# Performance work log

Hardware: AMD Instinct MI355X
Metric: run time of the kernel (lower is better)

## Reference

```python
import jax, jax.numpy as jnp
import numpy as np

N_QUBITS = 12
N_LAYERS = 3
N_PARAMS = N_QUBITS * 3 * N_LAYERS  # 108
BATCH = 8192
DIM = 1 << N_QUBITS  # 4096


def _rx(theta):
    c = jnp.cos(theta / 2).astype(jnp.complex64)
    s = jnp.sin(theta / 2).astype(jnp.complex64)
    return jnp.stack([jnp.stack([c, -1j * s]), jnp.stack([-1j * s, c])])


def _ry(theta):
    c = jnp.cos(theta / 2).astype(jnp.complex64)
    s = jnp.sin(theta / 2).astype(jnp.complex64)
    return jnp.stack([jnp.stack([c, -s]), jnp.stack([s, c])])


def _rz(theta):
    e = jnp.exp(-1j * theta.astype(jnp.complex64) / 2)
    z = jnp.zeros((), jnp.complex64)
    return jnp.stack([jnp.stack([e, z]), jnp.stack([z, jnp.conj(e)])])


def _apply_1q(state, q, U):
    # state: (B,) + (2,)*n ; apply 2x2 gate U on wire q (axis q+1)
    s = jnp.moveaxis(state, q + 1, -1)
    s = s @ U.T
    return jnp.moveaxis(s, -1, q + 1)


def _cnot(state, c, t):
    # control wire c, target wire t (axes offset by 1 for batch dim)
    ca, ta = c + 1, t + 1
    s0 = jax.lax.index_in_dim(state, 0, ca, keepdims=False)
    s1 = jax.lax.index_in_dim(state, 1, ca, keepdims=False)
    ta2 = ta - 1 if ta > ca else ta  # target axis shifts after removing control axis
    s1 = jnp.flip(s1, axis=ta2)  # X on target (size-2 axis)
    return jnp.stack([s0, s1], axis=ca)


def setup_inputs() -> dict:
    key = jax.random.key(0)
    k1, k2 = jax.random.split(key)
    x = jax.random.normal(k1, (BATCH, DIM), dtype=jnp.float32)
    params = jax.random.normal(k2, (N_PARAMS,), dtype=jnp.float32) * 0.1
    return {"x": x, "params": params}


def reference(x, params):
    n = N_QUBITS
    B = x.shape[0]
    # AmplitudeEmbedding with normalize=True
    norm = jnp.linalg.norm(x, axis=1, keepdims=True)
    state = (x / norm).astype(jnp.complex64).reshape((B,) + (2,) * n)
    idx = 0
    for _ in range(N_LAYERS):
        for q in range(n):
            state = _apply_1q(state, q, _rx(params[idx])); idx += 1
            state = _apply_1q(state, q, _ry(params[idx])); idx += 1
            state = _apply_1q(state, q, _rz(params[idx])); idx += 1
        for q in range(n):
            state = _cnot(state, q, (q + 1) % n)
    # <Z_q> = P(q=0) - P(q=1)
    p = state.real ** 2 + state.imag ** 2  # (B,) + (2,)*n, float32
    outs = []
    for q in range(n):
        axes = tuple(a for a in range(1, n + 1) if a != q + 1)
        marg = jnp.sum(p, axis=axes)  # (B, 2)
        outs.append(marg[:, 0] - marg[:, 1])
    return jnp.stack(outs, axis=1)  # (B, n_qubits)
```

## Files before the change

### kernel.cpp

```cpp
#include <hip/hip_runtime.h>
#include <math.h>

#define NQ 12
#define DIM 4096
#define NGATES 36
#define NROUND 9

typedef float f32x4 __attribute__((ext_vector_type(4)));
typedef __fp16 fp16x2 __attribute__((ext_vector_type(2)));
typedef __fp16 fp16x4 __attribute__((ext_vector_type(4)));
typedef __fp16 fp16x8 __attribute__((ext_vector_type(8)));

constexpr unsigned swz(unsigned x) { return x ^ (x >> 4); }
constexpr int pc(unsigned x) { int c = 0; while (x) { c += (int)(x & 1u); x >>= 1; } return c; }

constexpr bool rank4(const unsigned* v, int n) {
  unsigned pivs[4] = {0, 0, 0, 0};
  int rk = 0;
  for (int i = 0; i < n; ++i) {
    unsigned x = v[i] & 15u;
    for (int bit = 3; bit >= 0; --bit) {
      if (!((x >> bit) & 1u)) continue;
      if (pivs[bit]) x ^= pivs[bit];
      else { pivs[bit] = x; ++rk; break; }
    }
  }
  return rk == 4;
}

struct Round {
  unsigned s[4];
  unsigned gidx[4];
  unsigned colD[4];
  unsigned waveD[2];
  unsigned cbsw8[16];
  unsigned dt[4];
};
struct PlanT {
  Round rd[NROUND];
  unsigned zsel[NQ];
};

constexpr PlanT make_plan() {
  PlanT P{};
  unsigned Mcol[NQ] = {}, Minv[NQ] = {};
  for (int i = 0; i < NQ; ++i) { Mcol[i] = 1u << i; Minv[i] = 1u << i; }
  unsigned gm[NGATES] = {}, gs[NGATES] = {};
  int g = 0;
  for (int L = 0; L < 3; ++L) {
    for (int q = 0; q < NQ; ++q) { int b = NQ - 1 - q; gm[g] = Mcol[b]; gs[g] = Minv[b]; ++g; }
    for (int q = 0; q < NQ; ++q) {
      int bc = NQ - 1 - q, bt = NQ - 1 - ((q + 1) % NQ);
      Mcol[bc] ^= Mcol[bt];
      Minv[bt] ^= Minv[bc];
    }
  }
  for (int r = 0; r < NROUND; ++r) {
    unsigned m0[4], sl0[4];
    for (int k = 0; k < 4; ++k) { m0[k] = gm[4*r+k]; sl0[k] = gs[4*r+k]; }
    unsigned red[4];
    for (int k = 0; k < 4; ++k) red[k] = m0[k];
    for (int a = 0; a < 4; ++a) {
      unsigned pp = red[a] & (0u - red[a]);
      for (int b = a + 1; b < 4; ++b) if (red[b] & pp) red[b] ^= red[a];
    }
    unsigned piv[4];
    for (int a = 0; a < 4; ++a) piv[a] = red[a] & (0u - red[a]);
    for (int a = 0; a < 4; ++a)
      for (int b = a + 1; b < 4; ++b)
        if (piv[a] > piv[b]) { unsigned tp = piv[a]; piv[a] = piv[b]; piv[b] = tp; }
    unsigned l[4];
    for (int a = 0; a < 4; ++a) l[a] = piv[a] - 1u;
    unsigned D[8];
    for (int i = 0; i < 8; ++i) {
      unsigned j = 1u << i;
      j = ((j & ~l[0]) << 1) | (j & l[0]);
      j = ((j & ~l[1]) << 1) | (j & l[1]);
      j = ((j & ~l[2]) << 1) | (j & l[2]);
      j = ((j & ~l[3]) << 1) | (j & l[3]);
      D[i] = j;
    }
    const int gp[3][4] = {{0,1,2,3},{0,2,1,3},{0,3,1,2}};
    int bp = -1; unsigned bS = 0;
    for (int p = 0; p < 3 && bp < 0; ++p) {
      unsigned mm[4], ss[4];
      for (int k = 0; k < 4; ++k) { mm[k] = m0[gp[p][k]]; ss[k] = sl0[gp[p][k]]; }
      unsigned cbu[16];
      for (int d = 0; d < 16; ++d) {
        unsigned c = 0;
        for (int k = 0; k < 4; ++k) if ((d >> k) & 1) c ^= mm[k];
        cbu[d] = swz(c);
      }
      for (unsigned S = 0; S < 256 && bp < 0; ++S) {
        if (pc(S) != 4) continue;
        unsigned v[6]; int vi = 0;
        for (int i = 0; i < 8; ++i) if ((S >> i) & 1) {
          unsigned av = swz(D[i]);
          for (int k = 0; k < 4; ++k) if (pc(D[i] & ss[k]) & 1) av ^= cbu[1u << k];
          v[vi++] = av;
        }
        v[4] = cbu[4]; v[5] = cbu[8];
        if (rank4(v, 6)) { bp = p; bS = S; }
      }
    }
    if (bp < 0) { bp = 0; bS = 0x0Fu; }
    unsigned mm[4];
    for (int k = 0; k < 4; ++k) {
      P.rd[r].gidx[k] = (unsigned)gp[bp][k];
      P.rd[r].s[k]    = sl0[gp[bp][k]];
      mm[k]           = m0[gp[bp][k]];
    }
    unsigned cbu[16];
    for (int d = 0; d < 16; ++d) {
      unsigned c = 0;
      for (int k = 0; k < 4; ++k) if ((d >> k) & 1) c ^= mm[k];
      cbu[d] = swz(c);
      P.rd[r].cbsw8[d] = cbu[d] << 3;
    }
    unsigned cD[4], TD[2], WD[2];
    int nc = 0, other[4]; int no = 0;
    for (int i = 0; i < 8; ++i) {
      if ((bS >> i) & 1) cD[nc++] = D[i];
      else other[no++] = i;
    }
    TD[0] = D[other[0]]; TD[1] = D[other[1]];
    WD[0] = D[other[2]]; WD[1] = D[other[3]];
    for (int k = 0; k < 4; ++k) P.rd[r].colD[k] = cD[k];
    P.rd[r].waveD[0] = WD[0]; P.rd[r].waveD[1] = WD[1];
    for (int tt = 0; tt < 4; ++tt) {
      unsigned jt = ((tt & 1) ? TD[0] : 0u) ^ ((tt & 2) ? TD[1] : 0u);
      unsigned d8 = swz(jt);
      for (int k = 0; k < 4; ++k) if (pc(jt & P.rd[r].s[k]) & 1) d8 ^= cbu[1u << k];
      P.rd[r].dt[tt] = d8 << 3;
    }
  }
  for (int q = 0; q < NQ; ++q) P.zsel[q] = Minv[NQ - 1 - q];
  return P;
}

constexpr PlanT PLAN = make_plan();

__global__ void qc_prep(const float* __restrict__ params, __fp16* __restrict__ amat) {
  int t = threadIdx.x;
  int r = t >> 4, s = t & 15;
  if (r >= NROUND) return;
  float U[4][8];
  for (int k = 0; k < 4; ++k) {
    int gg = r * 4 + (int)PLAN.rd[r].gidx[k];
    float h1 = params[3*gg+0]*0.5f, hh2 = params[3*gg+1]*0.5f, h3 = params[3*gg+2]*0.5f;
    float c1 = cosf(h1), s1 = sinf(h1);
    float c2 = cosf(hh2), s2 = sinf(hh2);
    float c3 = cosf(h3), s3 = sinf(h3);
    float a00r =  c2*c1, a00i =  s2*s1;
    float a01r = -s2*c1, a01i = -c2*s1;
    float a10r =  s2*c1, a10i = -c2*s1;
    float a11r =  c2*c1, a11i = -s2*s1;
    U[k][0] = c3*a00r + s3*a00i;  U[k][1] = c3*a00i - s3*a00r;
    U[k][2] = c3*a01r + s3*a01i;  U[k][3] = c3*a01i - s3*a01r;
    U[k][4] = c3*a10r - s3*a10i;  U[k][5] = c3*a10i + s3*a10r;
    U[k][6] = c3*a11r - s3*a11i;  U[k][7] = c3*a11i + s3*a11r;
  }
  __fp16* b0 = amat + r*2048 + s*32;
  __fp16* b1 = b0 + 512;
  __fp16* b2 = b0 + 1024;
  __fp16* b3 = b0 + 1536;
  for (int j = 0; j < 16; ++j) {
    float pr = 1.f, pi = 0.f;
    for (int k = 0; k < 4; ++k) {
      int idx = ((((s >> k) & 1) * 2) + ((j >> k) & 1)) * 2;
      float gr = U[k][idx], gi = U[k][idx + 1];
      float npr = pr * gr - pi * gi;
      pi = pr * gi + pi * gr;
      pr = npr;
    }
    float v0_ =  pr; __fp16 e0 = (__fp16)v0_;
    float v1_ = -pi; __fp16 e1 = (__fp16)v1_;
    float v2_ =  pi; __fp16 e2 = (__fp16)v2_;
    float v3_ =  pr; __fp16 e3 = (__fp16)v3_;
    b0[2*j]   = e0;  b1[2*j]   = (__fp16)(v0_ - (float)e0);
    b0[2*j+1] = e1;  b1[2*j+1] = (__fp16)(v1_ - (float)e1);
    b2[2*j]   = e2;  b3[2*j]   = (__fp16)(v2_ - (float)e2);
    b2[2*j+1] = e3;  b3[2*j+1] = (__fp16)(v3_ - (float)e3);
  }
}

__global__ __launch_bounds__(256)
__attribute__((amdgpu_waves_per_eu(4, 5)))
void qc_main(const float* __restrict__ x, const __fp16* __restrict__ amat,
             float* __restrict__ out) {
  __shared__ float2 sst[DIM];
  char* sb = (char*)sst;
  const int t = threadIdx.x;
  const long row = blockIdx.x;

  const float4* x4 = (const float4*)(x + (size_t)row * DIM);
  float ssq = 0.f;
#pragma unroll
  for (int k = 0; k < 4; ++k) {
    float4 a = x4[t + 256*k];
    int j0 = 4*(t + 256*k);
    *(float2*)(sb + (swz((unsigned)j0)     << 3)) = make_float2(a.x, 0.f);
    *(float2*)(sb + (swz((unsigned)(j0+1)) << 3)) = make_float2(a.y, 0.f);
    *(float2*)(sb + (swz((unsigned)(j0+2)) << 3)) = make_float2(a.z, 0.f);
    *(float2*)(sb + (swz((unsigned)(j0+3)) << 3)) = make_float2(a.w, 0.f);
    ssq += a.x*a.x + a.y*a.y + a.z*a.z + a.w*a.w;
  }
#pragma unroll
  for (int off = 32; off > 0; off >>= 1) ssq += __shfl_down(ssq, off, 64);
  __syncthreads();

#pragma unroll 1
  for (int r = 0; r < NROUND; ++r) {
    const unsigned s0 = PLAN.rd[r].s[0], sA = PLAN.rd[r].s[1];
    const unsigned sB = PLAN.rd[r].s[2], sC = PLAN.rd[r].s[3];
    const unsigned cD0 = PLAN.rd[r].colD[0], cD1 = PLAN.rd[r].colD[1];
    const unsigned cD2 = PLAN.rd[r].colD[2], cD3 = PLAN.rd[r].colD[3];
    const unsigned W0 = PLAN.rd[r].waveD[0], W1 = PLAN.rd[r].waveD[1];
    const unsigned CB1 = PLAN.rd[r].cbsw8[1], CB2 = PLAN.rd[r].cbsw8[2];
    const unsigned CB3 = PLAN.rd[r].cbsw8[3];
    const unsigned C4 = PLAN.rd[r].cbsw8[4], C8 = PLAN.rd[r].cbsw8[8];
    const unsigned dts[4] = {0u, PLAN.rd[r].dt[1], PLAN.rd[r].dt[2], PLAN.rd[r].dt[3]};

    unsigned j = 0;
    j ^= (unsigned)(-(int)((t >> 0) & 1)) & cD0;
    j ^= (unsigned)(-(int)((t >> 1) & 1)) & cD1;
    j ^= (unsigned)(-(int)((t >> 2) & 1)) & cD2;
    j ^= (unsigned)(-(int)((t >> 3) & 1)) & cD3;
    j ^= (unsigned)(-(int)((t >> 6) & 1)) & W0;
    j ^= (unsigned)(-(int)((t >> 7) & 1)) & W1;
    unsigned adj8 = 0;
    adj8 ^= (unsigned)(-(int)(__popc(j & s0) & 1)) & CB1;
    adj8 ^= (unsigned)(-(int)(__popc(j & sA) & 1)) & CB2;
    adj8 ^= (unsigned)(-(int)(__popc(j & sB) & 1)) & C4;
    adj8 ^= (unsigned)(-(int)(__popc(j & sC) & 1)) & C8;
    const unsigned q = ((unsigned)t >> 4) & 3u;
    const unsigned qsel = ((q & 1u) ? C4 : 0u) ^ ((q & 2u) ? C8 : 0u);
    const unsigned b0a = (((j ^ (j >> 4)) << 3) ^ adj8) ^ qsel;

    const fp16x8* am = (const fp16x8*)(amat + (size_t)r * 2048);
    const int fo = (t & 15) * 4 + (int)q;
    const fp16x8 Arh = am[fo];
    const fp16x8 Arl = am[64 + fo];
    const fp16x8 Aih = am[128 + fo];
    const fp16x8 Ail = am[192 + fo];

#pragma unroll
    for (int tt = 0; tt < 4; ++tt) {
      const unsigned bb = b0a ^ dts[tt];
      const unsigned a0 = bb, a1 = bb ^ CB1, a2 = bb ^ CB2, a3 = bb ^ CB3;
      const float2 A0 = *(const float2*)(sb + a0);
      const float2 A1 = *(const float2*)(sb + a1);
      const float2 A2 = *(const float2*)(sb + a2);
      const float2 A3 = *(const float2*)(sb + a3);
      fp16x2 p0 = __builtin_amdgcn_cvt_pkrtz(A0.x, A0.y);
      fp16x2 p1 = __builtin_amdgcn_cvt_pkrtz(A1.x, A1.y);
      fp16x2 p2 = __builtin_amdgcn_cvt_pkrtz(A2.x, A2.y);
      fp16x2 p3 = __builtin_amdgcn_cvt_pkrtz(A3.x, A3.y);
      fp16x2 q0 = __builtin_amdgcn_cvt_pkrtz(A0.x - (float)p0[0], A0.y - (float)p0[1]);
      fp16x2 q1 = __builtin_amdgcn_cvt_pkrtz(A1.x - (float)p1[0], A1.y - (float)p1[1]);
      fp16x2 q2 = __builtin_amdgcn_cvt_pkrtz(A2.x - (float)p2[0], A2.y - (float)p2[1]);
      fp16x2 q3 = __builtin_amdgcn_cvt_pkrtz(A3.x - (float)p3[0], A3.y - (float)p3[1]);
      fp16x4 u01 = __builtin_shufflevector(p0, p1, 0, 1, 2, 3);
      fp16x4 u23 = __builtin_shufflevector(p2, p3, 0, 1, 2, 3);
      fp16x8 Bhi = __builtin_shufflevector(u01, u23, 0, 1, 2, 3, 4, 5, 6, 7);
      fp16x4 w01 = __builtin_shufflevector(q0, q1, 0, 1, 2, 3);
      fp16x4 w23 = __builtin_shufflevector(q2, q3, 0, 1, 2, 3);
      fp16x8 Blo = __builtin_shufflevector(w01, w23, 0, 1, 2, 3, 4, 5, 6, 7);

      f32x4 are = {0.f, 0.f, 0.f, 0.f}, aim = {0.f, 0.f, 0.f, 0.f};
      are = __builtin_amdgcn_mfma_f32_16x16x32_f16(Arh, Bhi, are, 0, 0, 0);
      are = __builtin_amdgcn_mfma_f32_16x16x32_f16(Arl, Bhi, are, 0, 0, 0);
      are = __builtin_amdgcn_mfma_f32_16x16x32_f16(Arh, Blo, are, 0, 0, 0);
      aim = __builtin_amdgcn_mfma_f32_16x16x32_f16(Aih, Bhi, aim, 0, 0, 0);
      aim = __builtin_amdgcn_mfma_f32_16x16x32_f16(Ail, Bhi, aim, 0, 0, 0);
      aim = __builtin_amdgcn_mfma_f32_16x16x32_f16(Aih, Blo, aim, 0, 0, 0);

      *(float2*)(sb + a0) = make_float2(are[0], aim[0]);
      *(float2*)(sb + a1) = make_float2(are[1], aim[1]);
      *(float2*)(sb + a2) = make_float2(are[2], aim[2]);
      *(float2*)(sb + a3) = make_float2(are[3], aim[3]);
    }
    __syncthreads();
  }

  const unsigned mbase8 = (((16u * (unsigned)t) ^ (unsigned)t) << 3);
  float p[16];
#pragma unroll
  for (int c = 0; c < 16; ++c) {
    float2 v = *(const float2*)(sb + (mbase8 ^ ((unsigned)c << 3)));
    p[c] = v.x * v.x + v.y * v.y;
  }
#pragma unroll
  for (int b = 0; b < 4; ++b) {
#pragma unroll
    for (int c = 0; c < 16; ++c) {
      if (!(c & (1 << b))) {
        const int c1 = c | (1 << b);
        float u = p[c], v = p[c1];
        p[c] = u + v; p[c1] = u - v;
      }
    }
  }
  float zs[NQ];
#pragma unroll
  for (int qq = 0; qq < NQ; ++qq) {
    const unsigned m = PLAN.zsel[qq];
    const float v = p[m & 15u];
    const int sgn = __popc((unsigned)t & (m >> 4)) & 1;
    zs[qq] = sgn ? -v : v;
  }

  __syncthreads();
#pragma unroll
  for (int k = 0; k < 6; ++k)
    *(float2*)(sb + (((unsigned)(k << 8) + (unsigned)t) << 3)) =
        make_float2(zs[2*k], zs[2*k+1]);
  if ((t & 63) == 0) *(float*)(sb + 12288 + (t >> 6) * 4) = ssq;
  __syncthreads();
  if (t < 192) {
    const int k = t >> 5, j = t & 31;
    const char* cbp = sb + (k << 11) + (j << 3);
    float2 acc = *(const float2*)(cbp);
#pragma unroll
    for (int i = 1; i < 8; ++i) {
      float2 vv = *(const float2*)(cbp + i * 256);
      acc.x += vv.x; acc.y += vv.y;
    }
#pragma unroll
    for (int off = 16; off > 0; off >>= 1) {
      acc.x += __shfl_down(acc.x, off, 32);
      acc.y += __shfl_down(acc.y, off, 32);
    }
    if (j == 0) *(float2*)(sb + 12352 + (k << 3)) = acc;
  }
  __syncthreads();
  if (t < NQ) {
    const float* sq = (const float*)(sb + 12288);
    const float den = sq[0] + sq[1] + sq[2] + sq[3];
    out[row * NQ + t] = ((const float*)(sb + 12352))[t] / den;
  }
}

extern "C" void kernel_launch(void* const* d_in, const int* in_sizes, int n_in,
                              void* d_out, int out_size, void* d_ws, size_t ws_size,
                              hipStream_t stream) {
  const float* x = (const float*)d_in[0];
  const float* params = (const float*)d_in[1];
  float* out = (float*)d_out;
  __fp16* amat = (__fp16*)d_ws;
  const int nrows = in_sizes[0] / DIM;
  qc_prep<<<dim3(1), dim3(256), 0, stream>>>(params, amat);
  qc_main<<<dim3(nrows), dim3(256), 0, stream>>>(x, amat, out);
}
```

Measured before the change: 305.0 us.

## Pair gate rounds into shared subspaces to drop every other block barrier

The compile-time plan now groups the nine 4-qubit gate rounds into pairs. Each pair's index decompositions span a common 10-dimensional subspace, with the same two wave-selecting directions for both rounds. Each wave therefore touches only its own slice of shared memory across both rounds of a pair, so the __syncthreads after even rounds can be removed. A constexpr verification with static_assert checks the span and bijectivity conditions; if they were wrong, the skipped barriers would create races.

```diff
diff --git a/kernel.cpp b/kernel.cpp
--- a/kernel.cpp
+++ b/kernel.cpp
@@ -13,6 +13,20 @@
 
 constexpr unsigned swz(unsigned x) { return x ^ (x >> 4); }
 constexpr int pc(unsigned x) { int c = 0; while (x) { c += (int)(x & 1u); x >>= 1; } return c; }
+constexpr int topbit(unsigned x) { int b = -1; while (x) { ++b; x >>= 1; } return b; }
+
+struct Ech {
+  unsigned piv[12] = {};
+  constexpr unsigned reduce(unsigned x) const {
+    while (x) { int b = topbit(x); if (!piv[b]) break; x ^= piv[b]; }
+    return x;
+  }
+  constexpr bool add(unsigned x) {
+    x = reduce(x); if (!x) return false; piv[topbit(x)] = x; return true;
+  }
+  constexpr bool contains(unsigned x) const { return reduce(x) == 0u; }
+  constexpr int dim() const { int d = 0; for (int i = 0; i < 12; ++i) if (piv[i]) ++d; return d; }
+};
 
 constexpr bool rank4(const unsigned* v, int n) {
   unsigned pivs[4] = {0, 0, 0, 0};
@@ -30,8 +44,8 @@
 
 struct Round {
   unsigned s[4];
-  unsigned gidx[4];
   unsigned colD[4];
+  unsigned tD[2];
   unsigned waveD[2];
   unsigned cbsw8[16];
   unsigned dt[4];
@@ -39,6 +53,7 @@
 struct PlanT {
   Round rd[NROUND];
   unsigned zsel[NQ];
+  bool ok;
 };
 
 constexpr PlanT make_plan() {
@@ -55,90 +70,107 @@
       Minv[bt] ^= Minv[bc];
     }
   }
-  for (int r = 0; r < NROUND; ++r) {
-    unsigned m0[4], sl0[4];
-    for (int k = 0; k < 4; ++k) { m0[k] = gm[4*r+k]; sl0[k] = gs[4*r+k]; }
-    unsigned red[4];
-    for (int k = 0; k < 4; ++k) red[k] = m0[k];
-    for (int a = 0; a < 4; ++a) {
-      unsigned pp = red[a] & (0u - red[a]);
-      for (int b = a + 1; b < 4; ++b) if (red[b] & pp) red[b] ^= red[a];
-    }
-    unsigned piv[4];
-    for (int a = 0; a < 4; ++a) piv[a] = red[a] & (0u - red[a]);
-    for (int a = 0; a < 4; ++a)
-      for (int b = a + 1; b < 4; ++b)
-        if (piv[a] > piv[b]) { unsigned tp = piv[a]; piv[a] = piv[b]; piv[b] = tp; }
-    unsigned l[4];
-    for (int a = 0; a < 4; ++a) l[a] = piv[a] - 1u;
-    unsigned D[8];
-    for (int i = 0; i < 8; ++i) {
-      unsigned j = 1u << i;
-      j = ((j & ~l[0]) << 1) | (j & l[0]);
-      j = ((j & ~l[1]) << 1) | (j & l[1]);
-      j = ((j & ~l[2]) << 1) | (j & l[2]);
-      j = ((j & ~l[3]) << 1) | (j & l[3]);
-      D[i] = j;
-    }
-    const int gp[3][4] = {{0,1,2,3},{0,2,1,3},{0,3,1,2}};
-    int bp = -1; unsigned bS = 0;
-    for (int p = 0; p < 3 && bp < 0; ++p) {
-      unsigned mm[4], ss[4];
-      for (int k = 0; k < 4; ++k) { mm[k] = m0[gp[p][k]]; ss[k] = sl0[gp[p][k]]; }
-      unsigned cbu[16];
+
+  for (int pr = 0; pr < 5; ++pr) {
+    const int r0 = 2 * pr;
+    const int nr = (pr == 4) ? 1 : 2;
+    Ech U{};
+    for (int rr = 0; rr < nr; ++rr)
+      for (int k = 0; k < 4; ++k) U.add(gm[4 * (r0 + rr) + k]);
+    unsigned pad[12] = {}; int npad = 0;
+    for (int i = 0; i < 12 && U.dim() < 10; ++i)
+      if (U.add(1u << i)) pad[npad++] = 1u << i;
+    Ech F = U;
+    unsigned Wv[2] = {}; int nw = 0;
+    for (int i = 0; i < 12 && nw < 2; ++i)
+      if (F.add(1u << i)) Wv[nw++] = 1u << i;
+
+    for (int rr = 0; rr < nr; ++rr) {
+      const int r = r0 + rr;
+      unsigned m[4], sl[4];
+      for (int k = 0; k < 4; ++k) {
+        m[k] = gm[4 * r + k]; sl[k] = gs[4 * r + k];
+        P.rd[r].s[k] = sl[k];
+      }
+      unsigned cbu[16] = {};
       for (int d = 0; d < 16; ++d) {
         unsigned c = 0;
-        for (int k = 0; k < 4; ++k) if ((d >> k) & 1) c ^= mm[k];
+        for (int k = 0; k < 4; ++k) if ((d >> k) & 1) c ^= m[k];
         cbu[d] = swz(c);
-      }
-      for (unsigned S = 0; S < 256 && bp < 0; ++S) {
-        if (pc(S) != 4) continue;
+        P.rd[r].cbsw8[d] = cbu[d] << 3;
+      }
+      Ech C{};
+      for (int k = 0; k < 4; ++k) C.add(m[k]);
+      unsigned comp[8] = {}; int nc = 0;
+      for (int rr2 = 0; rr2 < nr; ++rr2) {
+        if (rr2 == rr) continue;
+        for (int k = 0; k < 4; ++k) {
+          unsigned cand = gm[4 * (r0 + rr2) + k];
+          if (nc < 6 && C.add(cand)) comp[nc++] = cand;
+        }
+      }
+      for (int i = 0; i < npad && nc < 6; ++i)
+        if (C.add(pad[i])) comp[nc++] = pad[i];
+      unsigned av[6] = {};
+      for (int i = 0; i < 6; ++i) {
+        unsigned a = swz(comp[i]);
+        for (int k = 0; k < 4; ++k) if (pc(comp[i] & sl[k]) & 1) a ^= cbu[1u << k];
+        av[i] = a;
+      }
+      int bestmask = -1;
+      for (int sm = 0; sm < 64 && bestmask < 0; ++sm) {
+        if (pc((unsigned)sm) != 4) continue;
         unsigned v[6]; int vi = 0;
-        for (int i = 0; i < 8; ++i) if ((S >> i) & 1) {
-          unsigned av = swz(D[i]);
-          for (int k = 0; k < 4; ++k) if (pc(D[i] & ss[k]) & 1) av ^= cbu[1u << k];
-          v[vi++] = av;
-        }
+        for (int i = 0; i < 6; ++i) if ((sm >> i) & 1) v[vi++] = av[i];
         v[4] = cbu[4]; v[5] = cbu[8];
-        if (rank4(v, 6)) { bp = p; bS = S; }
-      }
-    }
-    if (bp < 0) { bp = 0; bS = 0x0Fu; }
-    unsigned mm[4];
-    for (int k = 0; k < 4; ++k) {
-      P.rd[r].gidx[k] = (unsigned)gp[bp][k];
-      P.rd[r].s[k]    = sl0[gp[bp][k]];
-      mm[k]           = m0[gp[bp][k]];
-    }
-    unsigned cbu[16];
-    for (int d = 0; d < 16; ++d) {
-      unsigned c = 0;
-      for (int k = 0; k < 4; ++k) if ((d >> k) & 1) c ^= mm[k];
-      cbu[d] = swz(c);
-      P.rd[r].cbsw8[d] = cbu[d] << 3;
-    }
-    unsigned cD[4], TD[2], WD[2];
-    int nc = 0, other[4]; int no = 0;
-    for (int i = 0; i < 8; ++i) {
-      if ((bS >> i) & 1) cD[nc++] = D[i];
-      else other[no++] = i;
-    }
-    TD[0] = D[other[0]]; TD[1] = D[other[1]];
-    WD[0] = D[other[2]]; WD[1] = D[other[3]];
-    for (int k = 0; k < 4; ++k) P.rd[r].colD[k] = cD[k];
-    P.rd[r].waveD[0] = WD[0]; P.rd[r].waveD[1] = WD[1];
-    for (int tt = 0; tt < 4; ++tt) {
-      unsigned jt = ((tt & 1) ? TD[0] : 0u) ^ ((tt & 2) ? TD[1] : 0u);
-      unsigned d8 = swz(jt);
-      for (int k = 0; k < 4; ++k) if (pc(jt & P.rd[r].s[k]) & 1) d8 ^= cbu[1u << k];
-      P.rd[r].dt[tt] = d8 << 3;
+        if (rank4(v, 6)) bestmask = sm;
+      }
+      if (bestmask < 0) bestmask = 0x0F;
+      int ci = 0, ti = 0;
+      for (int i = 0; i < 6; ++i) {
+        if ((bestmask >> i) & 1) { if (ci < 4) P.rd[r].colD[ci++] = comp[i]; }
+        else { if (ti < 2) P.rd[r].tD[ti++] = comp[i]; }
+      }
+      P.rd[r].waveD[0] = Wv[0]; P.rd[r].waveD[1] = Wv[1];
+      for (int tt = 0; tt < 4; ++tt) {
+        unsigned jt = ((tt & 1) ? P.rd[r].tD[0] : 0u) ^ ((tt & 2) ? P.rd[r].tD[1] : 0u);
+        unsigned d8 = swz(jt);
+        for (int k = 0; k < 4; ++k) if (pc(jt & sl[k]) & 1) d8 ^= cbu[1u << k];
+        P.rd[r].dt[tt] = d8 << 3;
+      }
     }
   }
   for (int q = 0; q < NQ; ++q) P.zsel[q] = Minv[NQ - 1 - q];
+
+  bool ok = true;
+  for (int pr = 0; pr < 5; ++pr) {
+    const int r0 = 2 * pr; const int nr = (pr == 4) ? 1 : 2;
+    for (int rr = 0; rr < nr; ++rr) {
+      const int r = r0 + rr;
+      Ech B{};
+      for (int k = 0; k < 4; ++k) ok = ok && B.add(gm[4 * r + k]);
+      for (int k = 0; k < 4; ++k) ok = ok && B.add(P.rd[r].colD[k]);
+      ok = ok && B.add(P.rd[r].tD[0]) && B.add(P.rd[r].tD[1]);
+      ok = ok && B.add(P.rd[r].waveD[0]) && B.add(P.rd[r].waveD[1]);
+      ok = ok && (B.dim() == 12);
+    }
+    if (nr == 2) {
+      Ech S{};
+      for (int k = 0; k < 4; ++k) S.add(gm[4 * r0 + k]);
+      for (int k = 0; k < 4; ++k) S.add(P.rd[r0].colD[k]);
+      S.add(P.rd[r0].tD[0]); S.add(P.rd[r0].tD[1]);
+      const int b = r0 + 1;
+      for (int k = 0; k < 4; ++k) ok = ok && S.contains(gm[4 * b + k]);
+      for (int k = 0; k < 4; ++k) ok = ok && S.contains(P.rd[b].colD[k]);
+      ok = ok && S.contains(P.rd[b].tD[0]) && S.contains(P.rd[b].tD[1]);
+    }
+  }
+  P.ok = ok;
   return P;
 }
 
 constexpr PlanT PLAN = make_plan();
+static_assert(PLAN.ok, "plan span/bijectivity conditions violated");
 
 __global__ void qc_prep(const float* __restrict__ params, __fp16* __restrict__ amat) {
   int t = threadIdx.x;
@@ -146,7 +178,7 @@
   if (r >= NROUND) return;
   float U[4][8];
   for (int k = 0; k < 4; ++k) {
-    int gg = r * 4 + (int)PLAN.rd[r].gidx[k];
+    int gg = r * 4 + k;
     float h1 = params[3*gg+0]*0.5f, hh2 = params[3*gg+1]*0.5f, h3 = params[3*gg+2]*0.5f;
     float c1 = cosf(h1), s1 = sinf(h1);
     float c2 = cosf(hh2), s2 = sinf(hh2);
@@ -280,7 +312,7 @@
       *(float2*)(sb + a2) = make_float2(are[2], aim[2]);
       *(float2*)(sb + a3) = make_float2(are[3], aim[3]);
     }
-    __syncthreads();
+    if ((r & 1) != 0 || r == NROUND - 1) __syncthreads();
   }
 
   const unsigned mbase8 = (((16u * (unsigned)t) ^ (unsigned)t) << 3);
```

Result: slower. 369.4 us (+21.1%).
